# Optimization experiments

Hardware: AMD Instinct MI355X
Metric: run time of the kernel (lower is better)

## Reference

```python
import jax, jax.numpy as jnp
import numpy as np


def setup_inputs() -> dict:
    key = jax.random.key(0)
    k1, k2, k3 = jax.random.split(key, 3)
    B, C, H, W = 64, 512, 28, 28
    K = 32
    std = 1.0 / (K * C) ** 0.5
    x = jax.random.normal(k1, (B, C, H, W), dtype=jnp.float32)
    codewords = jax.random.uniform(k2, (K, C), dtype=jnp.float32, minval=-std, maxval=std)
    scale = jax.random.uniform(k3, (K,), dtype=jnp.float32, minval=-1.0, maxval=0.0)
    return {"x": x, "codewords": codewords, "scale": scale}


def reference(x, codewords, scale):
    # x: (B, C, H, W) -> descriptors (B, N, C)
    B, C, H, W = x.shape
    K = codewords.shape[0]
    xd = x.reshape(B, C, H * W).transpose(0, 2, 1)  # (B, N, C)

    # scaled L2: scale_k * ||x_n - c_k||^2, expanded without (B,N,K,C) intermediate
    x_sq = jnp.sum(xd * xd, axis=-1, keepdims=True)            # (B, N, 1)
    c_sq = jnp.sum(codewords * codewords, axis=-1)             # (K,)
    xc = jnp.einsum("bnc,kc->bnk", xd, codewords)              # (B, N, K)
    dist = scale * (x_sq - 2.0 * xc + c_sq)                    # (B, N, K)

    A = jax.nn.softmax(dist, axis=2)                           # (B, N, K)

    # encoded_k = sum_n A[b,n,k] * (x[b,n] - c[k])
    wx = jnp.einsum("bnk,bnc->bkc", A, xd)                     # (B, K, C)
    wsum = jnp.sum(A, axis=1)                                  # (B, K)
    encoded = wx - wsum[:, :, None] * codewords[None, :, :]    # (B, K, C)
    return encoded
```

## Files before the change

### kernel.cpp

```cpp
#include <hip/hip_runtime.h>

#define BB 64
#define CC 512
#define NPIX 784
#define KK 32
#define NSA 49
#define AS 800
#define NSTEP 24

typedef __attribute__((ext_vector_type(8))) short short8;
typedef __attribute__((ext_vector_type(4))) float floatx4;

__device__ __forceinline__ unsigned short f2bf(float f) {
    union { float f; unsigned u; } v; v.f = f;
    return (unsigned short)((v.u + 0x7FFFu + ((v.u >> 16) & 1u)) >> 16);
}
__device__ __forceinline__ short8 pack8(const float4& a, const float4& b) {
    short8 r;
    r[0] = (short)f2bf(a.x); r[1] = (short)f2bf(a.y);
    r[2] = (short)f2bf(a.z); r[3] = (short)f2bf(a.w);
    r[4] = (short)f2bf(b.x); r[5] = (short)f2bf(b.y);
    r[6] = (short)f2bf(b.z); r[7] = (short)f2bf(b.w);
    return r;
}

__global__ __launch_bounds__(256) void kA(const float* __restrict__ x,
                                          const float* __restrict__ cw,
                                          const float* __restrict__ scale,
                                          unsigned short* __restrict__ Ag)
{
    __shared__ __align__(16) float red[4][64][12];
    __shared__ float csq_p[8][KK];
    __shared__ float csq_l[KK];

    const int t    = threadIdx.x;
    const int lane = t & 63, w = t >> 6;
    const int col  = lane & 15, quad = lane >> 4;
    const int split = blockIdx.x, b = blockIdx.y;
    const int p0    = split * 16;

    {
        const int k = t & 31, part = t >> 5;
        const float* cp = cw + k * CC + part * 64;
        float s = 0.f;
#pragma unroll
        for (int i = 0; i < 16; ++i) {
            const float4 v = *(const float4*)&cp[i * 4];
            s += v.x * v.x + v.y * v.y + v.z * v.z + v.w * v.w;
        }
        csq_p[part][k] = s;
    }

    const float* xb = x + (size_t)b * CC * NPIX + p0 + col;
    floatx4 acc0 = {0.f, 0.f, 0.f, 0.f};
    floatx4 acc1 = {0.f, 0.f, 0.f, 0.f};
    float xsqp = 0.f;
#pragma unroll
    for (int i = 0; i < 4; ++i) {
        const int c0 = (w * 4 + i) * 32 + quad * 8;
        float va[8];
#pragma unroll
        for (int j = 0; j < 8; ++j) va[j] = xb[(size_t)(c0 + j) * NPIX];
        const float4 c0a = *(const float4*)&cw[col * CC + c0];
        const float4 c0b = *(const float4*)&cw[col * CC + c0 + 4];
        const float4 c1a = *(const float4*)&cw[(col + 16) * CC + c0];
        const float4 c1b = *(const float4*)&cw[(col + 16) * CC + c0 + 4];
        short8 a;
#pragma unroll
        for (int j = 0; j < 8; ++j) { xsqp += va[j] * va[j]; a[j] = (short)f2bf(va[j]); }
        acc0 = __builtin_amdgcn_mfma_f32_16x16x32_bf16(a, pack8(c0a, c0b), acc0, 0, 0, 0);
        acc1 = __builtin_amdgcn_mfma_f32_16x16x32_bf16(a, pack8(c1a, c1b), acc1, 0, 0, 0);
    }
    *(floatx4*)&red[w][lane][0] = acc0;
    *(floatx4*)&red[w][lane][4] = acc1;
    red[w][lane][8] = xsqp;
    __syncthreads();
    if (t < KK) {
        float s = 0.f;
#pragma unroll
        for (int p = 0; p < 8; ++p) s += csq_p[p][t];
        csq_l[t] = s;
    }
    __syncthreads();

    if (w == 0) {
        floatx4 A0 = *(const floatx4*)&red[0][lane][0];
        floatx4 A1 = *(const floatx4*)&red[0][lane][4];
        float xq = red[0][lane][8];
#pragma unroll
        for (int wv = 1; wv < 4; ++wv) {
            A0 += *(const floatx4*)&red[wv][lane][0];
            A1 += *(const floatx4*)&red[wv][lane][4];
            xq += red[wv][lane][8];
        }
        xq += __shfl_xor(xq, 16);
        xq += __shfl_xor(xq, 32);
        const float s0 = scale[col], s1 = scale[col + 16];
        const float q0 = csq_l[col], q1 = csq_l[col + 16];
        unsigned short* Ab = Ag + (size_t)b * KK * AS + p0;
#pragma unroll
        for (int r = 0; r < 4; ++r) {
            const float xqr = __shfl(xq, quad * 4 + r);
            const float d0 = s0 * (xqr + q0 - 2.f * A0[r]);
            const float d1 = s1 * (xqr + q1 - 2.f * A1[r]);
            float mx = fmaxf(d0, d1);
            mx = fmaxf(mx, __shfl_xor(mx, 1));
            mx = fmaxf(mx, __shfl_xor(mx, 2));
            mx = fmaxf(mx, __shfl_xor(mx, 4));
            mx = fmaxf(mx, __shfl_xor(mx, 8));
            const float e0 = __expf(d0 - mx), e1 = __expf(d1 - mx);
            float sm = e0 + e1;
            sm += __shfl_xor(sm, 1);
            sm += __shfl_xor(sm, 2);
            sm += __shfl_xor(sm, 4);
            sm += __shfl_xor(sm, 8);
            const float inv = 1.f / sm;
            Ab[col * AS + quad * 4 + r]        = f2bf(e0 * inv);
            Ab[(col + 16) * AS + quad * 4 + r] = f2bf(e1 * inv);
        }
    } else if (w == 1 && split == NSA - 1) {
        const short8 z = {0, 0, 0, 0, 0, 0, 0, 0};
        const int k = lane >> 1, off = (lane & 1) * 8;
        *(short8*)&Ag[(size_t)b * KK * AS + (size_t)k * AS + NPIX + off] = z;
    }
}

__global__ __launch_bounds__(256) void kB(const float* __restrict__ x,
                                          const float* __restrict__ cw,
                                          const unsigned short* __restrict__ Ag,
                                          float* __restrict__ out)
{
    __shared__ float wred[KK][8];
    __shared__ float wsum_l[KK];

    const int t    = threadIdx.x;
    const int lane = t & 63, w = t >> 6;
    const int col  = lane & 15, quad = lane >> 4;
    const int cch  = blockIdx.x, b = blockIdx.y;

    const unsigned short* Ab = Ag + (size_t)b * KK * AS;

    {
        const int k = t & 31, part = t >> 5;
        const unsigned* ap = (const unsigned*)(Ab + (size_t)k * AS) + part * 49;
        float s = 0.f;
#pragma unroll
        for (int i = 0; i < 49; ++i) {
            const unsigned u = ap[i];
            union { unsigned uu; float f; } lo, hi;
            lo.uu = u << 16; hi.uu = u & 0xffff0000u;
            s += lo.f + hi.f;
        }
        wred[k][part] = s;
    }

    const int c = cch * 64 + w * 16 + col;
    const float* xp = x + ((size_t)b * CC + c) * NPIX;
    const unsigned short* a0p = Ab + (size_t)col * AS;
    const unsigned short* a1p = Ab + (size_t)(col + 16) * AS;
    const int qo = quad * 8;

    floatx4 acc0 = {0.f, 0.f, 0.f, 0.f};
    floatx4 acc1 = {0.f, 0.f, 0.f, 0.f};
#pragma unroll 6
    for (int s = 0; s < NSTEP; ++s) {
        const int off = s * 32 + qo;
        const short8 av0 = *(const short8*)&a0p[off];
        const short8 av1 = *(const short8*)&a1p[off];
        const float4 xv0 = *(const float4*)&xp[off];
        const float4 xv1 = *(const float4*)&xp[off + 4];
        const short8 bv = pack8(xv0, xv1);
        acc0 = __builtin_amdgcn_mfma_f32_16x16x32_bf16(av0, bv, acc0, 0, 0, 0);
        acc1 = __builtin_amdgcn_mfma_f32_16x16x32_bf16(av1, bv, acc1, 0, 0, 0);
    }
    {
        const int off = NSTEP * 32 + qo;
        const short8 av0 = *(const short8*)&a0p[off];
        const short8 av1 = *(const short8*)&a1p[off];
        float4 xv0 = make_float4(0.f, 0.f, 0.f, 0.f);
        float4 xv1 = make_float4(0.f, 0.f, 0.f, 0.f);
        if (quad < 2) {
            xv0 = *(const float4*)&xp[off];
            xv1 = *(const float4*)&xp[off + 4];
        }
        const short8 bv = pack8(xv0, xv1);
        acc0 = __builtin_amdgcn_mfma_f32_16x16x32_bf16(av0, bv, acc0, 0, 0, 0);
        acc1 = __builtin_amdgcn_mfma_f32_16x16x32_bf16(av1, bv, acc1, 0, 0, 0);
    }

    __syncthreads();
    if (t < KK) {
        float s = 0.f;
#pragma unroll
        for (int p = 0; p < 8; ++p) s += wred[t][p];
        wsum_l[t] = s;
    }
    __syncthreads();

    float* ob = out + (size_t)b * KK * CC + c;
    const float* cp = cw + c;
#pragma unroll
    for (int r = 0; r < 4; ++r) {
        const int k0 = quad * 4 + r;
        ob[(size_t)k0 * CC]        = acc0[r] - wsum_l[k0]      * cp[(size_t)k0 * CC];
        ob[(size_t)(k0 + 16) * CC] = acc1[r] - wsum_l[k0 + 16] * cp[(size_t)(k0 + 16) * CC];
    }
}

extern "C" void kernel_launch(void* const* d_in, const int* in_sizes, int n_in,
                              void* d_out, int out_size, void* d_ws, size_t ws_size,
                              hipStream_t stream) {
    const float* x     = (const float*)d_in[0];
    const float* cw    = (const float*)d_in[1];
    const float* scale = (const float*)d_in[2];
    float* out = (float*)d_out;
    unsigned short* Ag = (unsigned short*)d_ws;

    kA<<<dim3(NSA, BB), dim3(256), 0, stream>>>(x, cw, scale, Ag);
    kB<<<dim3(8, BB), dim3(256), 0, stream>>>(x, cw, Ag, out);
}
```

Measured before the change: 221.2 us.

## Give each kA wave full-channel pixel tiles, stage codewords in LDS, precompute wsum

kA now has each wave own 16 pixels and reduce over all 512 channels itself. Previously four waves split the channel dimension and combined partial results through an LDS reduction. Each block stages the codewords once in LDS as bf16 and double-buffers the strided x loads. Blocks per batch drop from 49 to 13, and the last block overlaps earlier pixels. kA also writes per-block softmax column sums into the workspace, so kB no longer re-reads the A matrix to compute wsum. The trade-offs are fewer blocks for latency hiding, an extra 32 KB LDS staging step per block, and wsum summed from fp32 values rather than the bf16-rounded A.

Result: faster. 182.8 us (-17.4%).

```diff
diff --git a/kernel.cpp b/kernel.cpp
--- a/kernel.cpp
+++ b/kernel.cpp
@@ -4,16 +4,23 @@
 #define CC 512
 #define NPIX 784
 #define KK 32
-#define NSA 49
+#define NSA 13
 #define AS 800
+#define CW_S 520
 #define NSTEP 24
 
 typedef __attribute__((ext_vector_type(8))) short short8;
 typedef __attribute__((ext_vector_type(4))) float floatx4;
+typedef __attribute__((ext_vector_type(4))) unsigned short ushort4v;
+
+#define WSUM_OFF (BB * KK * AS)
 
 __device__ __forceinline__ unsigned short f2bf(float f) {
     union { float f; unsigned u; } v; v.f = f;
     return (unsigned short)((v.u + 0x7FFFu + ((v.u >> 16) & 1u)) >> 16);
+}
+__device__ __forceinline__ float bf2f(unsigned short h) {
+    union { unsigned u; float f; } v; v.u = ((unsigned)h) << 16; return v.f;
 }
 __device__ __forceinline__ short8 pack8(const float4& a, const float4& b) {
     short8 r;
@@ -24,104 +31,145 @@
     return r;
 }
 
-__global__ __launch_bounds__(256) void kA(const float* __restrict__ x,
-                                          const float* __restrict__ cw,
-                                          const float* __restrict__ scale,
-                                          unsigned short* __restrict__ Ag)
+__global__ __launch_bounds__(256, 4) void kA(const float* __restrict__ x,
+                                             const float* __restrict__ cw,
+                                             const float* __restrict__ scale,
+                                             unsigned short* __restrict__ Ag)
 {
-    __shared__ __align__(16) float red[4][64][12];
+    __shared__ __align__(16) unsigned short cs[KK * CW_S];
     __shared__ float csq_p[8][KK];
     __shared__ float csq_l[KK];
+    __shared__ float wredA[4][KK];
 
     const int t    = threadIdx.x;
     const int lane = t & 63, w = t >> 6;
     const int col  = lane & 15, quad = lane >> 4;
     const int split = blockIdx.x, b = blockIdx.y;
-    const int p0    = split * 16;
-
+    const int p0    = (split < 12) ? split * 64 : 720;
+
+    if (split == 0 && t < 64) {
+        const short8 z = {0, 0, 0, 0, 0, 0, 0, 0};
+        const int k = t >> 1, off = (t & 1) * 8;
+        *(short8*)&Ag[(size_t)b * KK * AS + (size_t)k * AS + NPIX + off] = z;
+    }
+
+#pragma unroll 4
+    for (int j = 0; j < 16; ++j) {
+        const int qidx = t + j * 256;
+        const int row = qidx >> 7, qc = qidx & 127;
+        const float4 v = *(const float4*)&cw[row * CC + qc * 4];
+        ushort4v p; p.x = f2bf(v.x); p.y = f2bf(v.y); p.z = f2bf(v.z); p.w = f2bf(v.w);
+        *(ushort4v*)&cs[row * CW_S + qc * 4] = p;
+    }
+    __syncthreads();
     {
         const int k = t & 31, part = t >> 5;
-        const float* cp = cw + k * CC + part * 64;
         float s = 0.f;
-#pragma unroll
-        for (int i = 0; i < 16; ++i) {
-            const float4 v = *(const float4*)&cp[i * 4];
-            s += v.x * v.x + v.y * v.y + v.z * v.z + v.w * v.w;
+        for (int i = 0; i < 64; ++i) {
+            const float v = bf2f(cs[k * CW_S + part * 64 + i]);
+            s += v * v;
         }
         csq_p[part][k] = s;
     }
-
-    const float* xb = x + (size_t)b * CC * NPIX + p0 + col;
+    __syncthreads();
+    if (t < KK) {
+        float s = 0.f;
+#pragma unroll
+        for (int p = 0; p < 8; ++p) s += csq_p[p][t];
+        csq_l[t] = s;
+    }
+    __syncthreads();
+
+    const float s0 = scale[col], s1 = scale[col + 16];
+    const float q0 = csq_l[col], q1 = csq_l[col + 16];
+
+    const int px = p0 + w * 16 + col;
+    const float* xb = x + (size_t)b * CC * NPIX + px;
+
     floatx4 acc0 = {0.f, 0.f, 0.f, 0.f};
     floatx4 acc1 = {0.f, 0.f, 0.f, 0.f};
     float xsqp = 0.f;
-#pragma unroll
-    for (int i = 0; i < 4; ++i) {
-        const int c0 = (w * 4 + i) * 32 + quad * 8;
-        float va[8];
-#pragma unroll
-        for (int j = 0; j < 8; ++j) va[j] = xb[(size_t)(c0 + j) * NPIX];
-        const float4 c0a = *(const float4*)&cw[col * CC + c0];
-        const float4 c0b = *(const float4*)&cw[col * CC + c0 + 4];
-        const float4 c1a = *(const float4*)&cw[(col + 16) * CC + c0];
-        const float4 c1b = *(const float4*)&cw[(col + 16) * CC + c0 + 4];
-        short8 a;
-#pragma unroll
-        for (int j = 0; j < 8; ++j) { xsqp += va[j] * va[j]; a[j] = (short)f2bf(va[j]); }
-        acc0 = __builtin_amdgcn_mfma_f32_16x16x32_bf16(a, pack8(c0a, c0b), acc0, 0, 0, 0);
-        acc1 = __builtin_amdgcn_mfma_f32_16x16x32_bf16(a, pack8(c1a, c1b), acc1, 0, 0, 0);
-    }
-    *(floatx4*)&red[w][lane][0] = acc0;
-    *(floatx4*)&red[w][lane][4] = acc1;
-    red[w][lane][8] = xsqp;
+    float va[8], vb[8];
+
+#pragma unroll
+    for (int j = 0; j < 8; ++j) va[j] = xb[(size_t)(quad * 8 + j) * NPIX];
+
+#pragma unroll
+    for (int kc = 0; kc < 16; kc += 2) {
+        {
+            const int cb = (kc + 1) * 32 + quad * 8;
+#pragma unroll
+            for (int j = 0; j < 8; ++j) vb[j] = xb[(size_t)(cb + j) * NPIX];
+        }
+        {
+#pragma unroll
+            for (int j = 0; j < 8; ++j) xsqp += va[j] * va[j];
+            short8 a;
+#pragma unroll
+            for (int j = 0; j < 8; ++j) a[j] = (short)f2bf(va[j]);
+            const int cb0 = kc * 32 + quad * 8;
+            const short8 b0 = *(const short8*)&cs[col * CW_S + cb0];
+            const short8 b1 = *(const short8*)&cs[(col + 16) * CW_S + cb0];
+            acc0 = __builtin_amdgcn_mfma_f32_16x16x32_bf16(a, b0, acc0, 0, 0, 0);
+            acc1 = __builtin_amdgcn_mfma_f32_16x16x32_bf16(a, b1, acc1, 0, 0, 0);
+        }
+        if (kc + 2 < 16) {
+            const int cb = (kc + 2) * 32 + quad * 8;
+#pragma unroll
+            for (int j = 0; j < 8; ++j) va[j] = xb[(size_t)(cb + j) * NPIX];
+        }
+        {
+#pragma unroll
+            for (int j = 0; j < 8; ++j) xsqp += vb[j] * vb[j];
+            short8 a;
+#pragma unroll
+            for (int j = 0; j < 8; ++j) a[j] = (short)f2bf(vb[j]);
+            const int cb1 = (kc + 1) * 32 + quad * 8;
+            const short8 b0 = *(const short8*)&cs[col * CW_S + cb1];
+            const short8 b1 = *(const short8*)&cs[(col + 16) * CW_S + cb1];
+            acc0 = __builtin_amdgcn_mfma_f32_16x16x32_bf16(a, b0, acc0, 0, 0, 0);
+            acc1 = __builtin_amdgcn_mfma_f32_16x16x32_bf16(a, b1, acc1, 0, 0, 0);
+        }
+    }
+
+    xsqp += __shfl_xor(xsqp, 16);
+    xsqp += __shfl_xor(xsqp, 32);
+
+    unsigned short* Ab = Ag + (size_t)b * KK * AS + p0 + w * 16;
+    float ts0 = 0.f, ts1 = 0.f;
+#pragma unroll
+    for (int r = 0; r < 4; ++r) {
+        const float xq = __shfl(xsqp, quad * 4 + r);
+        const float d0 = s0 * (xq + q0 - 2.f * acc0[r]);
+        const float d1 = s1 * (xq + q1 - 2.f * acc1[r]);
+        float mx = fmaxf(d0, d1);
+        mx = fmaxf(mx, __shfl_xor(mx, 1));
+        mx = fmaxf(mx, __shfl_xor(mx, 2));
+        mx = fmaxf(mx, __shfl_xor(mx, 4));
+        mx = fmaxf(mx, __shfl_xor(mx, 8));
+        const float e0 = __expf(d0 - mx), e1 = __expf(d1 - mx);
+        float sm = e0 + e1;
+        sm += __shfl_xor(sm, 1);
+        sm += __shfl_xor(sm, 2);
+        sm += __shfl_xor(sm, 4);
+        sm += __shfl_xor(sm, 8);
+        const float inv = 1.f / sm;
+        const float a0 = e0 * inv, a1 = e1 * inv;
+        Ab[col * AS + quad * 4 + r]        = f2bf(a0);
+        Ab[(col + 16) * AS + quad * 4 + r] = f2bf(a1);
+        ts0 += a0; ts1 += a1;
+    }
+
+    ts0 += __shfl_xor(ts0, 16); ts0 += __shfl_xor(ts0, 32);
+    ts1 += __shfl_xor(ts1, 16); ts1 += __shfl_xor(ts1, 32);
+    if (quad == 0) { wredA[w][col] = ts0; wredA[w][col + 16] = ts1; }
     __syncthreads();
     if (t < KK) {
-        float s = 0.f;
-#pragma unroll
-        for (int p = 0; p < 8; ++p) s += csq_p[p][t];
-        csq_l[t] = s;
-    }
-    __syncthreads();
-
-    if (w == 0) {
-        floatx4 A0 = *(const floatx4*)&red[0][lane][0];
-        floatx4 A1 = *(const floatx4*)&red[0][lane][4];
-        float xq = red[0][lane][8];
-#pragma unroll
-        for (int wv = 1; wv < 4; ++wv) {
-            A0 += *(const floatx4*)&red[wv][lane][0];
-            A1 += *(const floatx4*)&red[wv][lane][4];
-            xq += red[wv][lane][8];
-        }
-        xq += __shfl_xor(xq, 16);
-        xq += __shfl_xor(xq, 32);
-        const float s0 = scale[col], s1 = scale[col + 16];
-        const float q0 = csq_l[col], q1 = csq_l[col + 16];
-        unsigned short* Ab = Ag + (size_t)b * KK * AS + p0;
-#pragma unroll
-        for (int r = 0; r < 4; ++r) {
-            const float xqr = __shfl(xq, quad * 4 + r);
-            const float d0 = s0 * (xqr + q0 - 2.f * A0[r]);
-            const float d1 = s1 * (xqr + q1 - 2.f * A1[r]);
-            float mx = fmaxf(d0, d1);
-            mx = fmaxf(mx, __shfl_xor(mx, 1));
-            mx = fmaxf(mx, __shfl_xor(mx, 2));
-            mx = fmaxf(mx, __shfl_xor(mx, 4));
-            mx = fmaxf(mx, __shfl_xor(mx, 8));
-            const float e0 = __expf(d0 - mx), e1 = __expf(d1 - mx);
-            float sm = e0 + e1;
-            sm += __shfl_xor(sm, 1);
-            sm += __shfl_xor(sm, 2);
-            sm += __shfl_xor(sm, 4);
-            sm += __shfl_xor(sm, 8);
-            const float inv = 1.f / sm;
-            Ab[col * AS + quad * 4 + r]        = f2bf(e0 * inv);
-            Ab[(col + 16) * AS + quad * 4 + r] = f2bf(e1 * inv);
-        }
-    } else if (w == 1 && split == NSA - 1) {
-        const short8 z = {0, 0, 0, 0, 0, 0, 0, 0};
-        const int k = lane >> 1, off = (lane & 1) * 8;
-        *(short8*)&Ag[(size_t)b * KK * AS + (size_t)k * AS + NPIX + off] = z;
+        float s;
+        if (split < 12) s = wredA[0][t] + wredA[1][t] + wredA[2][t] + wredA[3][t];
+        else            s = wredA[3][t];
+        float* wsf = (float*)(Ag + WSUM_OFF);
+        wsf[(size_t)(split * BB + b) * KK + t] = s;
     }
 }
 
@@ -130,7 +178,6 @@
                                           const unsigned short* __restrict__ Ag,
                                           float* __restrict__ out)
 {
-    __shared__ float wred[KK][8];
     __shared__ float wsum_l[KK];
 
     const int t    = threadIdx.x;
@@ -140,18 +187,12 @@
 
     const unsigned short* Ab = Ag + (size_t)b * KK * AS;
 
-    {
-        const int k = t & 31, part = t >> 5;
-        const unsigned* ap = (const unsigned*)(Ab + (size_t)k * AS) + part * 49;
+    if (t < KK) {
+        const float* wsf = (const float*)(Ag + WSUM_OFF);
         float s = 0.f;
 #pragma unroll
-        for (int i = 0; i < 49; ++i) {
-            const unsigned u = ap[i];
-            union { unsigned uu; float f; } lo, hi;
-            lo.uu = u << 16; hi.uu = u & 0xffff0000u;
-            s += lo.f + hi.f;
-        }
-        wred[k][part] = s;
+        for (int sp = 0; sp < NSA; ++sp) s += wsf[(size_t)(sp * BB + b) * KK + t];
+        wsum_l[t] = s;
     }
 
     const int c = cch * 64 + w * 16 + col;
@@ -189,13 +230,6 @@
     }
 
     __syncthreads();
-    if (t < KK) {
-        float s = 0.f;
-#pragma unroll
-        for (int p = 0; p < 8; ++p) s += wred[t][p];
-        wsum_l[t] = s;
-    }
-    __syncthreads();
 
     float* ob = out + (size_t)b * KK * CC + c;
     const float* cp = cw + c;
```
